# Kernel optimization log

Measured on AMD Instinct MI355X. Metric: run time of the kernel, lower is better.

## Reference

```python
import jax, jax.numpy as jnp
from jax import lax
import numpy as np

VOCAB = 100000
EMB = 256
HID = 512          # bidirectional total
H = HID // 2       # per-direction hidden
TAGS = 12
START_IDX = 10
STOP_IDX = 11
B, S = 32, 256
NEG = -10000.0


def setup_inputs() -> dict:
    key = jax.random.key(0)
    ks = jax.random.split(key, 14)
    sc = 0.1
    sentences = jax.random.randint(ks[0], (B, S), 0, VOCAB)
    emb = jax.random.normal(ks[1], (VOCAB, EMB), jnp.float32) * sc
    wih_f = jax.random.normal(ks[2], (4 * H, EMB), jnp.float32) * sc
    whh_f = jax.random.normal(ks[3], (4 * H, H), jnp.float32) * sc
    bih_f = jax.random.normal(ks[4], (4 * H,), jnp.float32) * sc
    bhh_f = jax.random.normal(ks[5], (4 * H,), jnp.float32) * sc
    wih_b = jax.random.normal(ks[6], (4 * H, EMB), jnp.float32) * sc
    whh_b = jax.random.normal(ks[7], (4 * H, H), jnp.float32) * sc
    bih_b = jax.random.normal(ks[8], (4 * H,), jnp.float32) * sc
    bhh_b = jax.random.normal(ks[9], (4 * H,), jnp.float32) * sc
    w_out = jax.random.normal(ks[10], (TAGS, HID), jnp.float32) * sc
    b_out = jax.random.normal(ks[11], (TAGS,), jnp.float32) * sc
    transitions = jax.random.normal(ks[12], (TAGS, TAGS), jnp.float32)
    transitions = transitions.at[START_IDX, :].set(NEG)   # never transition into START
    transitions = transitions.at[:, STOP_IDX].set(NEG)    # never transition out of STOP
    return dict(sentences=sentences, emb=emb, wih_f=wih_f, whh_f=whh_f,
                bih_f=bih_f, bhh_f=bhh_f, wih_b=wih_b, whh_b=whh_b,
                bih_b=bih_b, bhh_b=bhh_b, w_out=w_out, b_out=b_out,
                transitions=transitions)


def _lstm_dir(x, wih, whh, bih, bhh, reverse):
    # x: [B,S,E]; PyTorch gate order i,f,g,o
    xg = jnp.einsum('bse,ge->bsg', x, wih) + bih + bhh  # [B,S,4H]
    h0 = jnp.zeros((x.shape[0], whh.shape[1]), x.dtype)
    c0 = jnp.zeros_like(h0)

    def step(carry, g_t):
        h, c = carry
        g = g_t + h @ whh.T
        i, f, gg, o = jnp.split(g, 4, axis=-1)
        c = jax.nn.sigmoid(f) * c + jax.nn.sigmoid(i) * jnp.tanh(gg)
        h = jax.nn.sigmoid(o) * jnp.tanh(c)
        return (h, c), h

    _, hs = lax.scan(step, (h0, c0), jnp.swapaxes(xg, 0, 1), reverse=reverse)
    return jnp.swapaxes(hs, 0, 1)  # [B,S,H]


def _features(sentences, emb, wih_f, whh_f, bih_f, bhh_f,
              wih_b, whh_b, bih_b, bhh_b, w_out, b_out):
    x = emb[sentences]                                   # [B,S,E]
    hf = _lstm_dir(x, wih_f, whh_f, bih_f, bhh_f, False)
    hb = _lstm_dir(x, wih_b, whh_b, bih_b, bhh_b, True)
    h = jnp.concatenate([hf, hb], axis=-1)               # [B,S,HID]
    return jnp.einsum('bsh,th->bst', h, w_out) + b_out   # [B,S,TAGS]


def _viterbi(feats, transitions):
    # feats: [B,S,T]; returns (score [B], path [B,S] int32)
    T = feats.shape[-1]
    init = jnp.full((T,), NEG, feats.dtype).at[START_IDX].set(0.0)

    def step(fv, emit):
        scores = fv[None, :] + transitions               # [next_tag, prev_tag]
        bp = jnp.argmax(scores, axis=1).astype(jnp.int32)
        fv_new = jnp.max(scores, axis=1) + emit
        return fv_new, bp

    def per_seq(feat_seq):                               # [S,T]
        fv, bps = lax.scan(step, init, feat_seq)         # bps: [S,T]
        term = fv + transitions[STOP_IDX]
        best = jnp.argmax(term).astype(jnp.int32)
        score = term[best]

        def back(tag, bp_t):
            return bp_t[tag], tag

        _, path = lax.scan(back, best, bps, reverse=True)
        return score, path

    return jax.vmap(per_seq)(feats)


def reference(sentences, emb, wih_f, whh_f, bih_f, bhh_f,
              wih_b, whh_b, bih_b, bhh_b, w_out, b_out, transitions):
    feats = _features(sentences, emb, wih_f, whh_f, bih_f, bhh_f,
                      wih_b, whh_b, bih_b, bhh_b, w_out, b_out)
    score, path = _viterbi(feats, transitions)
    return score, path
```

## Files before the change

kernel.cpp:

```cpp
#include <hip/hip_runtime.h>
#include <math.h>

#define BATCH 32
#define SEQ 256
#define EMBD 256
#define HDIM 256
#define G4H 1024
#define TAGS 12
#define START_IDX 10
#define STOP_IDX 11
#define NEGV -10000.0f

#define KRES 16
#define KLDS_G 18
#define KSTR_G 42

#define WS_XG    0
#define WS_X     16777216
#define WS_WPACK 18874368
#define WS_HALL  19234816
#define WS_FEATS 23429120

__device__ __forceinline__ float bcast(float v, int l) {
    return __int_as_float(__builtin_amdgcn_readlane(__float_as_int(v), l));
}

__global__ void gather_x(const int* __restrict__ sent, const float* __restrict__ emb,
                         float* __restrict__ x) {
    int m = blockIdx.x;
    int lane = threadIdx.x;
    long long row = sent[m];
    float4 v = *(const float4*)(emb + row * EMBD + lane * 4);
    *(float4*)(x + (size_t)m * EMBD + lane * 4) = v;
}

__global__ void pack_whh(const float* __restrict__ whh_f, const float* __restrict__ whh_b,
                         float4* __restrict__ pack) {
    int idx = blockIdx.x * 256 + threadIdx.x;
    if (idx >= 2 * 2 * KSTR_G * 512) return;
    int g = idx & 511;
    int r = idx >> 9;
    int j = r % KSTR_G; r /= KSTR_G;
    int half = r & 1, dir = r >> 1;
    int R = (g >> 7) * 256 + half * 128 + (g & 127);
    const float* w = dir ? whh_b : whh_f;
    pack[idx] = *(const float4*)(w + (size_t)R * HDIM + KRES + 4 * KLDS_G + 4 * j);
}

__launch_bounds__(256)
__global__ void gemm_xg(const float* __restrict__ x,
                        const float* __restrict__ wih_f, const float* __restrict__ wih_b,
                        const float* __restrict__ bih_f, const float* __restrict__ bhh_f,
                        const float* __restrict__ bih_b, const float* __restrict__ bhh_b,
                        float* __restrict__ xg) {
    __shared__ __align__(16) float as[8][128];
    __shared__ __align__(16) float bs[8][128];
    int m0 = blockIdx.x * 128;
    int n0 = blockIdx.y * 128;
    int tid = threadIdx.x;
    int tx = tid & 15, ty = tid >> 4;
    int lr = tid >> 1;
    int lh = (tid & 1) * 4;

    const float* arow = x + (size_t)(m0 + lr) * EMBD;
    const float* brow;
    {
        int n = n0 + lr;
        const float* w = (n < G4H) ? wih_f : wih_b;
        brow = w + (size_t)(n & 1023) * EMBD;
    }

    float acc[8][8];
    #pragma unroll
    for (int i = 0; i < 8; i++)
        #pragma unroll
        for (int j = 0; j < 8; j++) acc[i][j] = 0.f;

    for (int k0 = 0; k0 < EMBD; k0 += 8) {
        float4 av = *(const float4*)(arow + k0 + lh);
        float4 bv = *(const float4*)(brow + k0 + lh);
        __syncthreads();
        as[lh + 0][lr] = av.x; as[lh + 1][lr] = av.y; as[lh + 2][lr] = av.z; as[lh + 3][lr] = av.w;
        bs[lh + 0][lr] = bv.x; bs[lh + 1][lr] = bv.y; bs[lh + 2][lr] = bv.z; bs[lh + 3][lr] = bv.w;
        __syncthreads();
        #pragma unroll
        for (int kk = 0; kk < 8; kk++) {
            float4 a0 = *(const float4*)&as[kk][ty * 8];
            float4 a1 = *(const float4*)&as[kk][ty * 8 + 4];
            float4 b0 = *(const float4*)&bs[kk][tx * 8];
            float4 b1 = *(const float4*)&bs[kk][tx * 8 + 4];
            float a[8] = {a0.x, a0.y, a0.z, a0.w, a1.x, a1.y, a1.z, a1.w};
            float b[8] = {b0.x, b0.y, b0.z, b0.w, b1.x, b1.y, b1.z, b1.w};
            #pragma unroll
            for (int i = 0; i < 8; i++)
                #pragma unroll
                for (int j = 0; j < 8; j++) acc[i][j] += a[i] * b[j];
        }
    }

    int n = n0 + tx * 8;
    int dir = n >> 10, g0 = n & 1023;
    const float* bih = dir ? bih_b : bih_f;
    const float* bhh = dir ? bhh_b : bhh_f;
    float bi[8], bh[8];
    #pragma unroll
    for (int j = 0; j < 8; j++) { bi[j] = bih[g0 + j]; bh[j] = bhh[g0 + j]; }
    float* ob = xg + (size_t)dir * 8192 * G4H;
    #pragma unroll
    for (int i = 0; i < 8; i++) {
        int m = m0 + ty * 8 + i;
        float v[8];
        #pragma unroll
        for (int j = 0; j < 8; j++) v[j] = (acc[i][j] + bi[j]) + bh[j];
        *(float4*)(ob + (size_t)m * G4H + g0)     = make_float4(v[0], v[1], v[2], v[3]);
        *(float4*)(ob + (size_t)m * G4H + g0 + 4) = make_float4(v[4], v[5], v[6], v[7]);
    }
}

__global__ void zero_sync(float* __restrict__ hx, int* __restrict__ flags) {
    int i = blockIdx.x * 256 + threadIdx.x;
    if (i < 64 * 512) hx[i] = 0.f;
    if (i < 128) flags[i] = 0;
}

#define DOT4(W, K)                                              \
    a0 += (W).x * bcast(hv[((K) + 0) >> 6], ((K) + 0) & 63);    \
    a1 += (W).y * bcast(hv[((K) + 1) >> 6], ((K) + 1) & 63);    \
    a2 += (W).z * bcast(hv[((K) + 2) >> 6], ((K) + 2) & 63);    \
    a3 += (W).w * bcast(hv[((K) + 3) >> 6], ((K) + 3) & 63);

__launch_bounds__(512)
__global__ void lstm_rec(const float* __restrict__ xg,
                         const float* __restrict__ whh_f, const float* __restrict__ whh_b,
                         const float4* __restrict__ wpack,
                         float* __restrict__ h_all,
                         float* __restrict__ hx, int* __restrict__ flags) {
    int blk = blockIdx.x;
    int half = blk & 1;
    int chain = blk >> 1;
    int dir = chain & 1, b = chain >> 1;
    int g = threadIdx.x;
    int lane = g & 63;
    int unit0 = half * 128;
    int R = (g >> 7) * 256 + unit0 + (g & 127);

    const float* whh = dir ? whh_b : whh_f;
    const float4* wp = wpack + (size_t)(dir * 2 + half) * KSTR_G * 512 + g;
    const float* xgb = xg + (size_t)dir * 8192 * G4H + (size_t)b * SEQ * G4H + R;
    float* hxc = hx + chain * 512;
    int* own_flag = flags + chain * 2 + half;
    int* par_flag = flags + chain * 2 + (1 - half);

    __shared__ __align__(16) float4 wlds[KLDS_G * 512];
    __shared__ float gates[512];

    #pragma unroll
    for (int j = 0; j < KLDS_G; j++)
        wlds[j * 512 + g] = *(const float4*)(whh + (size_t)R * HDIM + KRES + j * 4);
    float4 wr[KRES / 4];
    #pragma unroll
    for (int i = 0; i < KRES / 4; i++)
        wr[i] = *(const float4*)(whh + (size_t)R * HDIM + i * 4);

    float c = 0.f;
    __syncthreads();

    for (int t = 0; t < SEQ; t++) {
        int s = dir ? (SEQ - 1 - t) : t;

        float xval = xgb[(size_t)s * G4H];
        float4 sb[4];
        #pragma unroll
        for (int p = 0; p < 4; p++) sb[p] = wp[(size_t)p * 512];

        if (t > 0) {
            if (g == 0)
                while (__hip_atomic_load(par_flag, __ATOMIC_ACQUIRE,
                                         __HIP_MEMORY_SCOPE_AGENT) < t) {}
            __syncthreads();
        }

        int rp = (t + 1) & 1;
        float hv[4];
        #pragma unroll
        for (int j = 0; j < 4; j++)
            hv[j] = __hip_atomic_load(hxc + rp * 256 + j * 64 + lane,
                                      __ATOMIC_RELAXED, __HIP_MEMORY_SCOPE_AGENT);

        float a0 = xval, a1 = 0.f, a2 = 0.f, a3 = 0.f;

        #pragma unroll
        for (int i = 0; i < KRES / 4; i++) {
            float4 w = wr[i];
            DOT4(w, i * 4)
        }
        #pragma unroll
        for (int j = 0; j < KLDS_G; j++) {
            float4 w = wlds[j * 512 + g];
            DOT4(w, KRES + j * 4)
        }
        #pragma unroll
        for (int j = 0; j < KSTR_G; j++) {
            float4 w = sb[j & 3];
            if (j + 4 < KSTR_G) sb[j & 3] = wp[(size_t)(j + 4) * 512];
            DOT4(w, KRES + 4 * KLDS_G + j * 4)
        }

        gates[g] = (a0 + a1) + (a2 + a3);
        __syncthreads();
        if (g < 128) {
            float gi = gates[g], gf = gates[128 + g], gg = gates[256 + g], go = gates[384 + g];
            float si = 1.f / (1.f + expf(-gi));
            float sf = 1.f / (1.f + expf(-gf));
            float so = 1.f / (1.f + expf(-go));
            c = sf * c + si * tanhf(gg);
            float h = so * tanhf(c);
            int u = unit0 + g;
            h_all[((size_t)b * SEQ + s) * 512 + dir * HDIM + u] = h;
            __hip_atomic_store(hxc + (t & 1) * 256 + u, h,
                               __ATOMIC_RELAXED, __HIP_MEMORY_SCOPE_AGENT);
        }
        __syncthreads();
        if (g == 0)
            __hip_atomic_store(own_flag, t + 1,
                               __ATOMIC_RELEASE, __HIP_MEMORY_SCOPE_AGENT);
    }
}

__global__ void feats_kernel(const float* __restrict__ h_all, const float* __restrict__ w_out,
                             const float* __restrict__ b_out, float* __restrict__ feats) {
    int p = blockIdx.x;
    int lane = threadIdx.x;
    const float* h = h_all + (size_t)p * 512;
    for (int f = 0; f < TAGS; f++) {
        float s = 0.f;
        const float* w = w_out + f * 512;
        #pragma unroll
        for (int k = 0; k < 512; k += 64) s += h[k + lane] * w[k + lane];
        #pragma unroll
        for (int off = 32; off; off >>= 1) s += __shfl_down(s, off);
        if (lane == 0) feats[(size_t)p * TAGS + f] = s + b_out[f];
    }
}

__global__ void viterbi_kernel(const float* __restrict__ feats, const float* __restrict__ trans,
                               float* __restrict__ out) {
    int b = blockIdx.x;
    int t = threadIdx.x;
    __shared__ float fv[TAGS], fvn[TAGS], tr[TAGS * TAGS];
    __shared__ int bp[SEQ][TAGS];

    for (int i = t; i < TAGS * TAGS; i += 64) tr[i] = trans[i];
    if (t < TAGS) fv[t] = (t == START_IDX) ? 0.f : NEGV;
    __syncthreads();

    const float* fb = feats + (size_t)b * SEQ * TAGS;
    for (int s = 0; s < SEQ; s++) {
        if (t < TAGS) {
            float best = fv[0] + tr[t * TAGS + 0];
            int bi = 0;
            #pragma unroll
            for (int prev = 1; prev < TAGS; prev++) {
                float v = fv[prev] + tr[t * TAGS + prev];
                if (v > best) { best = v; bi = prev; }
            }
            bp[s][t] = bi;
            fvn[t] = best + fb[s * TAGS + t];
        }
        __syncthreads();
        if (t < TAGS) fv[t] = fvn[t];
        __syncthreads();
    }

    if (t == 0) {
        float best = fv[0] + tr[STOP_IDX * TAGS + 0];
        int bi = 0;
        #pragma unroll
        for (int p = 1; p < TAGS; p++) {
            float v = fv[p] + tr[STOP_IDX * TAGS + p];
            if (v > best) { best = v; bi = p; }
        }
        out[b] = best;
        float* path = out + BATCH + (size_t)b * SEQ;
        int tag = bi;
        path[SEQ - 1] = (float)tag;
        for (int s = SEQ - 1; s >= 1; s--) {
            tag = bp[s][tag];
            path[s - 1] = (float)tag;
        }
    }
}

extern "C" void kernel_launch(void* const* d_in, const int* in_sizes, int n_in,
                              void* d_out, int out_size, void* d_ws, size_t ws_size,
                              hipStream_t stream) {
    const int*   sent  = (const int*)d_in[0];
    const float* emb   = (const float*)d_in[1];
    const float* wih_f = (const float*)d_in[2];
    const float* whh_f = (const float*)d_in[3];
    const float* bih_f = (const float*)d_in[4];
    const float* bhh_f = (const float*)d_in[5];
    const float* wih_b = (const float*)d_in[6];
    const float* whh_b = (const float*)d_in[7];
    const float* bih_b = (const float*)d_in[8];
    const float* bhh_b = (const float*)d_in[9];
    const float* w_out = (const float*)d_in[10];
    const float* b_out = (const float*)d_in[11];
    const float* trans = (const float*)d_in[12];
    float* ws    = (float*)d_ws;
    float* xg    = ws + WS_XG;
    float* x     = ws + WS_X;
    float* wpack = ws + WS_WPACK;
    float* h_all = ws + WS_HALL;
    float* feats = ws + WS_FEATS;
    float* hx    = ws + WS_X;
    int*   flags = (int*)(ws + WS_X + 64 * 512);
    float* out   = (float*)d_out;

    gather_x<<<BATCH * SEQ, 64, 0, stream>>>(sent, emb, x);
    pack_whh<<<(2 * 2 * KSTR_G * 512 + 255) / 256, 256, 0, stream>>>(whh_f, whh_b, (float4*)wpack);
    gemm_xg<<<dim3(64, 16), 256, 0, stream>>>(x, wih_f, wih_b, bih_f, bhh_f, bih_b, bhh_b, xg);
    zero_sync<<<128, 256, 0, stream>>>(hx, flags);
    lstm_rec<<<128, 512, 0, stream>>>(xg, whh_f, whh_b, (const float4*)wpack, h_all, hx, flags);
    feats_kernel<<<BATCH * SEQ, 64, 0, stream>>>(h_all, w_out, b_out, feats);
    viterbi_kernel<<<BATCH, 64, 0, stream>>>(feats, trans, out);
}
```

Baseline: 1.620 ms.

## Split each LSTM chain across four workgroups with K-split partial sums

The recurrent LSTM kernel now spreads each (batch, direction) chain over four workgroups instead of two, each owning 64 hidden units. Threads split the hidden-state reduction into two K halves that are summed through shared memory. This leaves far fewer weights streamed per thread from global memory, since KSTR_G drops from 42 to 10, and it uses 256 workgroups instead of 128. The cost is an extra barrier per step and a wait on three peer flags per step instead of one, which raises cross-workgroup sync latency on the serial critical path.

```diff
diff --git a/kernel.cpp b/kernel.cpp
--- a/kernel.cpp
+++ b/kernel.cpp
@@ -13,7 +13,7 @@
 
 #define KRES 16
 #define KLDS_G 18
-#define KSTR_G 42
+#define KSTR_G 10
 
 #define WS_XG    0
 #define WS_X     16777216
@@ -37,14 +37,15 @@
 __global__ void pack_whh(const float* __restrict__ whh_f, const float* __restrict__ whh_b,
                          float4* __restrict__ pack) {
     int idx = blockIdx.x * 256 + threadIdx.x;
-    if (idx >= 2 * 2 * KSTR_G * 512) return;
+    if (idx >= 2 * 4 * KSTR_G * 512) return;
     int g = idx & 511;
-    int r = idx >> 9;
-    int j = r % KSTR_G; r /= KSTR_G;
-    int half = r & 1, dir = r >> 1;
-    int R = (g >> 7) * 256 + half * 128 + (g & 127);
+    int r2 = idx >> 9;
+    int j = r2 % KSTR_G; r2 /= KSTR_G;
+    int q = r2 & 3, dir = r2 >> 2;
+    int R = ((g >> 6) & 3) * 256 + q * 64 + (g & 63);
+    int k = (g >> 8) * 128 + KRES + 4 * KLDS_G + 4 * j;
     const float* w = dir ? whh_b : whh_f;
-    pack[idx] = *(const float4*)(w + (size_t)R * HDIM + KRES + 4 * KLDS_G + 4 * j);
+    pack[idx] = *(const float4*)(w + (size_t)R * HDIM + k);
 }
 
 __launch_bounds__(256)
@@ -120,14 +121,14 @@
 __global__ void zero_sync(float* __restrict__ hx, int* __restrict__ flags) {
     int i = blockIdx.x * 256 + threadIdx.x;
     if (i < 64 * 512) hx[i] = 0.f;
-    if (i < 128) flags[i] = 0;
-}
-
-#define DOT4(W, K)                                              \
-    a0 += (W).x * bcast(hv[((K) + 0) >> 6], ((K) + 0) & 63);    \
-    a1 += (W).y * bcast(hv[((K) + 1) >> 6], ((K) + 1) & 63);    \
-    a2 += (W).z * bcast(hv[((K) + 2) >> 6], ((K) + 2) & 63);    \
-    a3 += (W).w * bcast(hv[((K) + 3) >> 6], ((K) + 3) & 63);
+    if (i < 64 * 4) flags[i] = 0;
+}
+
+#define DOT4(W, KL)                                              \
+    a0 += (W).x * bcast(hv[((KL) + 0) >> 6], ((KL) + 0) & 63);   \
+    a1 += (W).y * bcast(hv[((KL) + 1) >> 6], ((KL) + 1) & 63);   \
+    a2 += (W).z * bcast(hv[((KL) + 2) >> 6], ((KL) + 2) & 63);   \
+    a3 += (W).w * bcast(hv[((KL) + 3) >> 6], ((KL) + 3) & 63);
 
 __launch_bounds__(512)
 __global__ void lstm_rec(const float* __restrict__ xg,
@@ -136,31 +137,33 @@
                          float* __restrict__ h_all,
                          float* __restrict__ hx, int* __restrict__ flags) {
     int blk = blockIdx.x;
-    int half = blk & 1;
-    int chain = blk >> 1;
+    int chain = blk & 63;
+    int q = blk >> 6;
     int dir = chain & 1, b = chain >> 1;
     int g = threadIdx.x;
     int lane = g & 63;
-    int unit0 = half * 128;
-    int R = (g >> 7) * 256 + unit0 + (g & 127);
+    int r = g & 255;
+    int kh = g >> 8;
+    int G = r >> 6, ul = r & 63;
+    int R = G * 256 + q * 64 + ul;
 
     const float* whh = dir ? whh_b : whh_f;
-    const float4* wp = wpack + (size_t)(dir * 2 + half) * KSTR_G * 512 + g;
+    const float* wrow = whh + (size_t)R * HDIM + kh * 128;
+    const float4* wp = wpack + (size_t)(dir * 4 + q) * KSTR_G * 512 + g;
     const float* xgb = xg + (size_t)dir * 8192 * G4H + (size_t)b * SEQ * G4H + R;
     float* hxc = hx + chain * 512;
-    int* own_flag = flags + chain * 2 + half;
-    int* par_flag = flags + chain * 2 + (1 - half);
+    int* fl = flags + chain * 4;
 
     __shared__ __align__(16) float4 wlds[KLDS_G * 512];
-    __shared__ float gates[512];
+    __shared__ float part[512];
 
     #pragma unroll
     for (int j = 0; j < KLDS_G; j++)
-        wlds[j * 512 + g] = *(const float4*)(whh + (size_t)R * HDIM + KRES + j * 4);
+        wlds[j * 512 + g] = *(const float4*)(wrow + KRES + j * 4);
     float4 wr[KRES / 4];
     #pragma unroll
     for (int i = 0; i < KRES / 4; i++)
-        wr[i] = *(const float4*)(whh + (size_t)R * HDIM + i * 4);
+        wr[i] = *(const float4*)(wrow + i * 4);
 
     float c = 0.f;
     __syncthreads();
@@ -168,26 +171,29 @@
     for (int t = 0; t < SEQ; t++) {
         int s = dir ? (SEQ - 1 - t) : t;
 
-        float xval = xgb[(size_t)s * G4H];
+        float xval = 0.f;
+        if (g < 256) xval = xgb[(size_t)s * G4H];
         float4 sb[4];
         #pragma unroll
         for (int p = 0; p < 4; p++) sb[p] = wp[(size_t)p * 512];
 
         if (t > 0) {
-            if (g == 0)
-                while (__hip_atomic_load(par_flag, __ATOMIC_ACQUIRE,
+            if (g < 3) {
+                int pq = g + (g >= q ? 1 : 0);
+                while (__hip_atomic_load(fl + pq, __ATOMIC_ACQUIRE,
                                          __HIP_MEMORY_SCOPE_AGENT) < t) {}
+            }
             __syncthreads();
         }
 
         int rp = (t + 1) & 1;
-        float hv[4];
-        #pragma unroll
-        for (int j = 0; j < 4; j++)
-            hv[j] = __hip_atomic_load(hxc + rp * 256 + j * 64 + lane,
+        float hv[2];
+        #pragma unroll
+        for (int j = 0; j < 2; j++)
+            hv[j] = __hip_atomic_load(hxc + rp * 256 + kh * 128 + j * 64 + lane,
                                       __ATOMIC_RELAXED, __HIP_MEMORY_SCOPE_AGENT);
 
-        float a0 = xval, a1 = 0.f, a2 = 0.f, a3 = 0.f;
+        float a0 = 0.f, a1 = 0.f, a2 = 0.f, a3 = 0.f;
 
         #pragma unroll
         for (int i = 0; i < KRES / 4; i++) {
@@ -206,23 +212,25 @@
             DOT4(w, KRES + 4 * KLDS_G + j * 4)
         }
 
-        gates[g] = (a0 + a1) + (a2 + a3);
-        __syncthreads();
-        if (g < 128) {
-            float gi = gates[g], gf = gates[128 + g], gg = gates[256 + g], go = gates[384 + g];
+        part[g] = (a0 + a1) + (a2 + a3);
+        __syncthreads();
+        if (g < 256) part[g] = part[g] + part[g + 256] + xval;
+        __syncthreads();
+        if (g < 64) {
+            float gi = part[g], gf = part[64 + g], gg = part[128 + g], go = part[192 + g];
             float si = 1.f / (1.f + expf(-gi));
             float sf = 1.f / (1.f + expf(-gf));
             float so = 1.f / (1.f + expf(-go));
             c = sf * c + si * tanhf(gg);
             float h = so * tanhf(c);
-            int u = unit0 + g;
+            int u = q * 64 + g;
             h_all[((size_t)b * SEQ + s) * 512 + dir * HDIM + u] = h;
             __hip_atomic_store(hxc + (t & 1) * 256 + u, h,
                                __ATOMIC_RELAXED, __HIP_MEMORY_SCOPE_AGENT);
         }
         __syncthreads();
         if (g == 0)
-            __hip_atomic_store(own_flag, t + 1,
+            __hip_atomic_store(fl + q, t + 1,
                                __ATOMIC_RELEASE, __HIP_MEMORY_SCOPE_AGENT);
     }
 }
@@ -318,10 +326,10 @@
     float* out   = (float*)d_out;
 
     gather_x<<<BATCH * SEQ, 64, 0, stream>>>(sent, emb, x);
-    pack_whh<<<(2 * 2 * KSTR_G * 512 + 255) / 256, 256, 0, stream>>>(whh_f, whh_b, (float4*)wpack);
+    pack_whh<<<(2 * 4 * KSTR_G * 512 + 255) / 256, 256, 0, stream>>>(whh_f, whh_b, (float4*)wpack);
     gemm_xg<<<dim3(64, 16), 256, 0, stream>>>(x, wih_f, wih_b, bih_f, bhh_f, bih_b, bhh_b, xg);
     zero_sync<<<128, 256, 0, stream>>>(hx, flags);
-    lstm_rec<<<128, 512, 0, stream>>>(xg, whh_f, whh_b, (const float4*)wpack, h_all, hx, flags);
+    lstm_rec<<<256, 512, 0, stream>>>(xg, whh_f, whh_b, (const float4*)wpack, h_all, hx, flags);
     feats_kernel<<<BATCH * SEQ, 64, 0, stream>>>(h_all, w_out, b_out, feats);
     viterbi_kernel<<<BATCH, 64, 0, stream>>>(feats, trans, out);
 }
```

Result: slower. 1.776 ms (+9.6%).
